# Kernel tuning notes

Hardware: AMD Instinct MI355X
Metric: run time of the kernel (lower is better)

The kernel has to match this reference:

```python
import jax, jax.numpy as jnp
import numpy as np

D_MODEL = 1024
NUM_HEADS = 16
HEAD_DIM = D_MODEL // NUM_HEADS
THETA = 10000.0
B, T = 2, 2048


def setup_inputs() -> dict:
    key = jax.random.key(0)
    k1, k2, k3 = jax.random.split(key, 3)
    x = jax.random.normal(k1, (B, T, D_MODEL), dtype=jnp.float32)
    W_qkv = jax.random.normal(k2, (3 * D_MODEL, D_MODEL), dtype=jnp.float32) * 0.02
    W_o = jax.random.normal(k3, (D_MODEL, D_MODEL), dtype=jnp.float32) * 0.02
    return {"x": x, "W_qkv": W_qkv, "W_o": W_o}


def _rope(x, cos, sin):
    # x: [B, h, T, d]; rotate interleaved even/odd pairs
    x_even = x[..., 0::2]
    x_odd = x[..., 1::2]
    out_even = x_even * cos - x_odd * sin
    out_odd = x_even * sin + x_odd * cos
    out = jnp.stack([out_even, out_odd], axis=-1)  # [B,h,T,d/2,2]
    return out.reshape(x.shape)


def reference(x, W_qkv, W_o):
    b, t, dm = x.shape
    # fused QKV projection (bias-free Linear: x @ W.T)
    qkv = jnp.einsum('btd,ed->bte', x, W_qkv)                # [B,T,3*D]
    qkv = qkv.reshape(b, t, 3, NUM_HEADS, HEAD_DIM)
    qkv = jnp.transpose(qkv, (2, 0, 3, 1, 4))                # [3,B,h,T,d]
    q, k, v = qkv[0], qkv[1], qkv[2]

    # RoPE with token_positions = arange(T)
    pos = jnp.arange(t, dtype=jnp.float32)                   # [T]
    inv_freq = THETA ** (-jnp.arange(0, HEAD_DIM, 2, dtype=jnp.float32) / HEAD_DIM)
    ang = pos[:, None] * inv_freq[None, :]                   # [T, d/2]
    cos = jnp.cos(ang)[None, None, :, :]
    sin = jnp.sin(ang)[None, None, :, :]
    q = _rope(q, cos, sin)
    k = _rope(k, cos, sin)

    # causal scaled dot-product attention
    scale = 1.0 / jnp.sqrt(jnp.asarray(HEAD_DIM, dtype=x.dtype))
    scores = jnp.einsum('bhqd,bhkd->bhqk', q, k) * scale     # [B,h,T,T]
    causal = jnp.tril(jnp.ones((t, t), dtype=bool))
    scores = jnp.where(causal[None, None, :, :], scores, -jnp.inf)
    attn = jax.nn.softmax(scores, axis=-1)
    out = jnp.einsum('bhqk,bhkd->bhqd', attn, v)             # [B,h,T,d]
    out = jnp.transpose(out, (0, 2, 1, 3)).reshape(b, t, dm) # [B,T,D]
    return jnp.einsum('btd,ed->bte', out, W_o)
```

## Files before the change

### kernel.cpp

```cpp
#include <hip/hip_runtime.h>
#include <hip/hip_bf16.h>
#include <cstdint>

#define NHEADS 16
#define HDIM 64
#define BB 2
#define TSEQ 2048
#define DM 1024
#define MROWS (BB*TSEQ)

typedef unsigned short u16;
typedef unsigned int u32;
typedef __bf16 bf16x8 __attribute__((ext_vector_type(8)));
typedef float f32x4 __attribute__((ext_vector_type(4)));

#define AS1C(p) ((const __attribute__((address_space(1))) u32*)(p))
#define AS3(p)  ((__attribute__((address_space(3))) u32*)(p))

static __device__ __forceinline__ u16 f2bf(float f) {
  return __builtin_bit_cast(u16, __float2bfloat16(f));
}
static __device__ __forceinline__ float bf2f(u16 u) {
  return __bfloat162float(__builtin_bit_cast(__hip_bfloat16, u));
}
static __device__ __forceinline__ u32 pack2bf(float a, float b) {
  const u32 ua = __builtin_bit_cast(u32, a) + 0x8000u;
  const u32 ub = __builtin_bit_cast(u32, b) + 0x8000u;
  return (ua >> 16) | (ub & 0xFFFF0000u);
}
static __device__ __forceinline__ f32x4 mfma16x16(bf16x8 a, bf16x8 b, f32x4 c) {
  return __builtin_amdgcn_mfma_f32_16x16x32_bf16(a, b, c, 0, 0, 0);
}

#define N4_X   (MROWS * DM / 4)
#define N4_WQ  (3 * DM * DM / 4)
#define N4_WO  (DM * DM / 4)
__global__ __launch_bounds__(256) void cast_all(const float* __restrict__ x,
                                                const float* __restrict__ wq,
                                                const float* __restrict__ wo,
                                                u16* __restrict__ xb,
                                                u16* __restrict__ wqb,
                                                u16* __restrict__ wob) {
  int i = blockIdx.x * 256 + threadIdx.x;
  const int stride = gridDim.x * 256;
  for (; i < N4_X + N4_WQ + N4_WO; i += stride) {
    const float4* src; u16* dst; int j;
    if (i < N4_X)            { src = (const float4*)x;  dst = xb;  j = i; }
    else if (i < N4_X + N4_WQ) { src = (const float4*)wq; dst = wqb; j = i - N4_X; }
    else                     { src = (const float4*)wo; dst = wob; j = i - N4_X - N4_WQ; }
    float4 v = src[j];
    ushort4 o;
    o.x = f2bf(v.x); o.y = f2bf(v.y); o.z = f2bf(v.z); o.w = f2bf(v.w);
    ((ushort4*)dst)[j] = o;
  }
}

template<int WRITE_BF16>
__global__ __launch_bounds__(256, 2) void gemm_bt(const u16* __restrict__ A,
                                                  const u16* __restrict__ Bm,
                                                  float* __restrict__ Cf,
                                                  u16* __restrict__ Cb,
                                                  int M, int N, int K) {
  __shared__ u16 lA[2][128 * 32];
  __shared__ u16 lB[2][128 * 32];
  const int tid = threadIdx.x;
  const int w = tid >> 6, l = tid & 63;
  const int wr = w >> 1, wc = w & 1;
  int bid = blockIdx.y * gridDim.x + blockIdx.x;
  const int cpx = (gridDim.x * gridDim.y) >> 3;
  bid = (bid & 7) * cpx + (bid >> 3);
  const int bx = bid % gridDim.x, by = bid / gridDim.x;
  const int brow = by * 128, bcol = bx * 128;
  const int lr = l & 15, lg = l >> 4;

  const int srow = l >> 2;
  const int scol = (((l & 3) ^ (srow & 3)) * 8);

  auto stage = [&](int buf, int k0) {
#pragma unroll
    for (int is = 0; is < 2; ++is) {
      const int chunk = w * 2 + is;
      const int row = chunk * 16 + srow;
      __builtin_amdgcn_global_load_lds(AS1C(A + (size_t)(brow + row) * K + k0 + scol),
                                       AS3((char*)lA[buf] + chunk * 1024), 16, 0, 0);
      __builtin_amdgcn_global_load_lds(AS1C(Bm + (size_t)(bcol + row) * K + k0 + scol),
                                       AS3((char*)lB[buf] + chunk * 1024), 16, 0, 0);
    }
  };

  f32x4 acc[4][4] = {};
  const int nk = K >> 5;
  stage(0, 0);
  for (int kk = 0; kk < nk; ++kk) {
    const int cur = kk & 1;
    __syncthreads();
    if (kk + 1 < nk) stage(cur ^ 1, (kk + 1) << 5);
    bf16x8 af[4], bfr[4];
#pragma unroll
    for (int m = 0; m < 4; ++m) {
      const int row = wr * 64 + m * 16 + lr;
      const int sl = lg ^ (row & 3);
      af[m] = *(const bf16x8*)(&lA[cur][row * 32 + sl * 8]);
    }
#pragma unroll
    for (int n = 0; n < 4; ++n) {
      const int row = wc * 64 + n * 16 + lr;
      const int sl = lg ^ (row & 3);
      bfr[n] = *(const bf16x8*)(&lB[cur][row * 32 + sl * 8]);
    }
#pragma unroll
    for (int m = 0; m < 4; ++m)
#pragma unroll
      for (int n = 0; n < 4; ++n)
        acc[m][n] = mfma16x16(af[m], bfr[n], acc[m][n]);
  }
#pragma unroll
  for (int m = 0; m < 4; ++m)
#pragma unroll
    for (int n = 0; n < 4; ++n)
#pragma unroll
      for (int r = 0; r < 4; ++r) {
        const int row = brow + wr * 64 + m * 16 + lg * 4 + r;
        const int col = bcol + wc * 64 + n * 16 + lr;
        if constexpr (WRITE_BF16)
          Cb[(size_t)row * N + col] = f2bf(acc[m][n][r]);
        else
          Cf[(size_t)row * N + col] = acc[m][n][r];
      }
}

__global__ __launch_bounds__(256, 2) void gemm_bt64(const u16* __restrict__ A,
                                                    const u16* __restrict__ Bm,
                                                    float* __restrict__ Cf,
                                                    int M, int N, int K) {
  __shared__ u16 lA[2][64 * 32];
  __shared__ u16 lB[2][128 * 32];
  const int tid = threadIdx.x;
  const int w = tid >> 6, l = tid & 63;
  const int wr = w >> 1, wc = w & 1;
  int bid = blockIdx.y * gridDim.x + blockIdx.x;
  const int cpx = (gridDim.x * gridDim.y) >> 3;
  bid = (bid & 7) * cpx + (bid >> 3);
  const int bx = bid % gridDim.x, by = bid / gridDim.x;
  const int brow = by * 64, bcol = bx * 128;
  const int lr = l & 15, lg = l >> 4;

  const int srow = l >> 2;
  const int scol = (((l & 3) ^ (srow & 3)) * 8);

  auto stage = [&](int buf, int k0) {
    {
      const int row = w * 16 + srow;
      __builtin_amdgcn_global_load_lds(AS1C(A + (size_t)(brow + row) * K + k0 + scol),
                                       AS3((char*)lA[buf] + w * 1024), 16, 0, 0);
    }
#pragma unroll
    for (int is = 0; is < 2; ++is) {
      const int chunk = w * 2 + is;
      const int row = chunk * 16 + srow;
      __builtin_amdgcn_global_load_lds(AS1C(Bm + (size_t)(bcol + row) * K + k0 + scol),
                                       AS3((char*)lB[buf] + chunk * 1024), 16, 0, 0);
    }
  };

  f32x4 acc[2][4] = {};
  const int nk = K >> 5;
  stage(0, 0);
  for (int kk = 0; kk < nk; ++kk) {
    const int cur = kk & 1;
    __syncthreads();
    if (kk + 1 < nk) stage(cur ^ 1, (kk + 1) << 5);
    bf16x8 af[2], bfr[4];
#pragma unroll
    for (int m = 0; m < 2; ++m) {
      const int row = wr * 32 + m * 16 + lr;
      const int sl = lg ^ (row & 3);
      af[m] = *(const bf16x8*)(&lA[cur][row * 32 + sl * 8]);
    }
#pragma unroll
    for (int n = 0; n < 4; ++n) {
      const int row = wc * 64 + n * 16 + lr;
      const int sl = lg ^ (row & 3);
      bfr[n] = *(const bf16x8*)(&lB[cur][row * 32 + sl * 8]);
    }
#pragma unroll
    for (int m = 0; m < 2; ++m)
#pragma unroll
      for (int n = 0; n < 4; ++n)
        acc[m][n] = mfma16x16(af[m], bfr[n], acc[m][n]);
  }
#pragma unroll
  for (int m = 0; m < 2; ++m)
#pragma unroll
    for (int n = 0; n < 4; ++n)
#pragma unroll
      for (int r = 0; r < 4; ++r) {
        const int row = brow + wr * 32 + m * 16 + lg * 4 + r;
        const int col = bcol + wc * 64 + n * 16 + lr;
        Cf[(size_t)row * N + col] = acc[m][n][r];
      }
}

__global__ __launch_bounds__(256) void rope_reshape(const u16* __restrict__ qkvb,
                                                    u16* __restrict__ qb,
                                                    u16* __restrict__ kb,
                                                    u16* __restrict__ vbT) {
  const int bh = blockIdx.y;
  const int b = bh >> 4, h = bh & 15;
  const int t0 = blockIdx.x * 64;
  const int tid = threadIdx.x;
  const float C = -0.4152410118609203f;
  const float QS = 0.125f * 1.44269504088896341f;
  const float R2PI = 0.15915494309189535f;

  for (int idx = tid; idx < 64 * 8; idx += 256) {
    const int tl = idx >> 3, grp = idx & 7;
    const int t = t0 + tl;
    const size_t base = ((size_t)(b * TSEQ + t)) * 3072 + h * 64 + grp * 8;
    u16 qv[8], kv8[8], qo[8], ko[8];
    *(uint4*)qv  = *(const uint4*)(qkvb + base);
    *(uint4*)kv8 = *(const uint4*)(qkvb + base + 1024);
#pragma unroll
    for (int j = 0; j < 4; ++j) {
      const int p = grp * 4 + j;
      const float inv = exp2f((float)p * C);
      const float rev = __builtin_amdgcn_fractf((float)t * inv * R2PI);
      const float sn = __builtin_amdgcn_sinf(rev);
      const float cs = __builtin_amdgcn_cosf(rev);
      const float qe = bf2f(qv[2 * j]), qoo = bf2f(qv[2 * j + 1]);
      const float ke = bf2f(kv8[2 * j]), koo = bf2f(kv8[2 * j + 1]);
      qo[2 * j]     = f2bf((qe * cs - qoo * sn) * QS);
      qo[2 * j + 1] = f2bf((qe * sn + qoo * cs) * QS);
      ko[2 * j]     = f2bf(ke * cs - koo * sn);
      ko[2 * j + 1] = f2bf(ke * sn + koo * cs);
    }
    const size_t obase = ((size_t)bh * TSEQ + t) * 64 + grp * 8;
    *(uint4*)(qb + obase) = *(uint4*)qo;
    *(uint4*)(kb + obase) = *(uint4*)ko;
  }

  __shared__ u16 lT[64][65];
  for (int idx = tid; idx < 64 * 64; idx += 256) {
    const int tl = idx >> 6, d = idx & 63;
    lT[tl][d] = qkvb[((size_t)(b * TSEQ + t0 + tl)) * 3072 + 2048 + h * 64 + d];
  }
  __syncthreads();
  for (int idx = tid; idx < 64 * 64; idx += 256) {
    const int d = idx >> 6, tl = idx & 63;
    vbT[((size_t)bh * 64 + d) * TSEQ + t0 + tl] = lT[tl][d];
  }
}

__global__ __launch_bounds__(512, 4) void attn_fwd(const u16* __restrict__ qb,
                                                   const u16* __restrict__ kb,
                                                   const u16* __restrict__ vbT,
                                                   u16* __restrict__ ob) {
  __shared__ u16 lK[4][64 * 64];
  __shared__ u16 lV[4][64 * 64];
  __shared__ u16 lP[8][16 * 64];
  const int hw = blockIdx.x;
  const int logical = (hw & 7) * 64 + (hw >> 3);
  const int bh = logical >> 4;
  const int pair = logical & 15;
  const int b = bh >> 4, h = bh & 15;
  const int tid = threadIdx.x;
  const int w = tid >> 6, l = tid & 63;
  const int g = w >> 2, wq = w & 3;
  const int lr = l & 15, lg = l >> 4;
  const int srow8 = l >> 3;
  const int scol = ((l & 7) ^ srow8) * 8;
  const u16* Kb = kb + (size_t)bh * TSEQ * 64;
  const u16* Vb = vbT + (size_t)bh * 64 * TSEQ;
  u16* lPw = lP[w];

  auto stage = [&](int buf, int kt) {
#pragma unroll
    for (int is = 0; is < 2; ++is) {
      const int chunk = wq * 2 + is;
      const int row = chunk * 8 + srow8;
      __builtin_amdgcn_global_load_lds(AS1C(Kb + (size_t)(kt * 64 + row) * 64 + scol),
                                       AS3((char*)lK[buf] + chunk * 1024), 16, 0, 0);
      __builtin_amdgcn_global_load_lds(AS1C(Vb + (size_t)row * TSEQ + kt * 64 + scol),
                                       AS3((char*)lV[buf] + chunk * 1024), 16, 0, 0);
    }
  };

  for (int half = 0; half < 2; ++half) {
    const int qt = half ? (TSEQ / 64 - 1 - pair) : pair;
    const int q0 = qt * 64;

    bf16x8 qf[2];
    {
      const u16* qp = qb + ((size_t)bh * TSEQ + q0 + wq * 16 + lr) * 64 + lg * 8;
      qf[0] = *(const bf16x8*)qp;
      qf[1] = *(const bf16x8*)(qp + 32);
    }

    f32x4 oacc[4] = {};
    float lsum = 0.f;

    const int nt = qt + 1;
    const int nit = (nt + 1) >> 1;
    const int ql = wq * 16 + lr;

    __syncthreads();
    if (g < nt) stage(g * 2, g);
    for (int it = 0; it < nit; ++it) {
      const int cur = it & 1;
      __syncthreads();
      const int ktn = 2 * (it + 1) + g;
      if (ktn < nt) stage(g * 2 + (cur ^ 1), ktn);
      const int kt = 2 * it + g;
      if (kt < nt) {
        const u16* Kc = lK[g * 2 + cur];
        const u16* Vc = lV[g * 2 + cur];

        f32x4 s[4] = {};
        __builtin_amdgcn_s_setprio(1);
#pragma unroll
        for (int n = 0; n < 4; ++n) {
          const int row = n * 16 + lr;
#pragma unroll
          for (int ks = 0; ks < 2; ++ks) {
            const int sl = (ks * 4 + lg) ^ (row & 7);
            bf16x8 kf = *(const bf16x8*)(&Kc[row * 64 + sl * 8]);
            s[n] = mfma16x16(kf, qf[ks], s[n]);
          }
        }
        __builtin_amdgcn_s_setprio(0);

        const bool diag = (kt == qt);
#pragma unroll
        for (int n = 0; n < 4; ++n) {
          float pv[4];
#pragma unroll
          for (int r = 0; r < 4; ++r) {
            float p = __builtin_amdgcn_exp2f(s[n][r]);
            if (diag && (n * 16 + lg * 4 + r > ql)) p = 0.f;
            pv[r] = p;
            lsum += p;
          }
          const u32 w0 = pack2bf(pv[0], pv[1]);
          const u32 w1 = pack2bf(pv[2], pv[3]);
          const int phys = (n * 2 + (lg >> 1)) ^ (lr & 7);
          uint2 pk; pk.x = w0; pk.y = w1;
          *(uint2*)(&lPw[lr * 64 + phys * 8 + (lg & 1) * 4]) = pk;
        }

        bf16x8 pf[2];
#pragma unroll
        for (int ks = 0; ks < 2; ++ks) {
          const int phys = (ks * 4 + lg) ^ (lr & 7);
          pf[ks] = *(const bf16x8*)(&lPw[lr * 64 + phys * 8]);
        }
        __builtin_amdgcn_s_setprio(1);
#pragma unroll
        for (int n = 0; n < 4; ++n) {
          const int row = n * 16 + lr;
#pragma unroll
          for (int ks = 0; ks < 2; ++ks) {
            const int sl = (ks * 4 + lg) ^ (row & 7);
            bf16x8 vf = *(const bf16x8*)(&Vc[row * 64 + sl * 8]);
            oacc[n] = mfma16x16(vf, pf[ks], oacc[n]);
          }
        }
        __builtin_amdgcn_s_setprio(0);
      }
    }

    lsum += __shfl_xor(lsum, 16);
    lsum += __shfl_xor(lsum, 32);

    __syncthreads();
    float* mO = (float*)&lK[0][0];
    float* mL = (float*)&lV[0][0];
    if (g == 1) {
#pragma unroll
      for (int n = 0; n < 4; ++n)
#pragma unroll
        for (int r = 0; r < 4; ++r) {
          const int d = n * 16 + lg * 4 + r;
          mO[wq * 1024 + d * 16 + lr] = oacc[n][r];
        }
      if (lg == 0) mL[wq * 16 + lr] = lsum;
    }
    __syncthreads();
    if (g == 0) {
      const float rl = 1.f / (lsum + mL[wq * 16 + lr]);
      const int q = q0 + wq * 16 + lr;
#pragma unroll
      for (int n = 0; n < 4; ++n) {
        ushort4 ov;
#pragma unroll
        for (int r = 0; r < 4; ++r) {
          const int d = n * 16 + lg * 4 + r;
          const float o = oacc[n][r] + mO[wq * 1024 + d * 16 + lr];
          ((u16*)&ov)[r] = f2bf(o * rl);
        }
        *(ushort4*)(&ob[(size_t)(b * TSEQ + q) * DM + h * 64 + n * 16 + lg * 4]) = ov;
      }
    }
  }
}

extern "C" void kernel_launch(void* const* d_in, const int* in_sizes, int n_in,
                              void* d_out, int out_size, void* d_ws, size_t ws_size,
                              hipStream_t stream) {
  const float* x    = (const float*)d_in[0];
  const float* Wqkv = (const float*)d_in[1];
  const float* Wo   = (const float*)d_in[2];
  float* out = (float*)d_out;

  char* ws = (char*)d_ws;
  u16* xb    = (u16*)ws; ws += (size_t)MROWS * DM * 2;
  u16* wqkvb = (u16*)ws; ws += (size_t)3 * DM * DM * 2;
  u16* wob   = (u16*)ws; ws += (size_t)DM * DM * 2;
  u16* qkvb  = (u16*)ws; ws += (size_t)MROWS * 3 * DM * 2;
  u16* qb    = (u16*)ws; ws += (size_t)BB * NHEADS * TSEQ * HDIM * 2;
  u16* kb    = (u16*)ws; ws += (size_t)BB * NHEADS * TSEQ * HDIM * 2;
  u16* vbT   = (u16*)ws; ws += (size_t)BB * NHEADS * TSEQ * HDIM * 2;
  u16* ob    = (u16*)ws; ws += (size_t)MROWS * DM * 2;

  cast_all<<<2048, 256, 0, stream>>>(x, Wqkv, Wo, xb, wqkvb, wob);

  gemm_bt<1><<<dim3(3 * DM / 128, MROWS / 128), 256, 0, stream>>>(
      xb, wqkvb, nullptr, qkvb, MROWS, 3 * DM, DM);

  rope_reshape<<<dim3(TSEQ / 64, BB * NHEADS), 256, 0, stream>>>(qkvb, qb, kb, vbT);

  attn_fwd<<<512, 512, 0, stream>>>(qb, kb, vbT, ob);

  gemm_bt64<<<dim3(DM / 128, MROWS / 64), 256, 0, stream>>>(
      ob, wob, out, MROWS, DM, DM);
}
```

Baseline: 106.7 us.

## Fuse RoPE, head reshape and V transpose into QKV GEMM epilogue

The separate rope_reshape kernel and the intermediate qkv bf16 buffer are removed. The QKV GEMM epilogue now applies RoPE (with the softmax scale folded into Q) using a lane shuffle to fetch each pair partner, and writes Q and K directly in per-head layout. V is written transposed as packed 4-element stores. This saves one kernel launch and a full write/read round trip of the QKV tensor. In exchange the GEMM epilogue does more transcendental math and scattered stores, which lengthens the GEMM.

After: 100.6 us. 5.7% less time.

```diff
diff --git a/kernel.cpp b/kernel.cpp
--- a/kernel.cpp
+++ b/kernel.cpp
@@ -55,12 +55,12 @@
   }
 }
 
-template<int WRITE_BF16>
-__global__ __launch_bounds__(256, 2) void gemm_bt(const u16* __restrict__ A,
-                                                  const u16* __restrict__ Bm,
-                                                  float* __restrict__ Cf,
-                                                  u16* __restrict__ Cb,
-                                                  int M, int N, int K) {
+__global__ __launch_bounds__(256, 2) void gemm_qkv(const u16* __restrict__ A,
+                                                   const u16* __restrict__ Bm,
+                                                   u16* __restrict__ qb,
+                                                   u16* __restrict__ kbuf,
+                                                   u16* __restrict__ vbT,
+                                                   int M, int N, int K) {
   __shared__ u16 lA[2][128 * 32];
   __shared__ u16 lB[2][128 * 32];
   const int tid = threadIdx.x;
@@ -114,19 +114,52 @@
       for (int n = 0; n < 4; ++n)
         acc[m][n] = mfma16x16(af[m], bfr[n], acc[m][n]);
   }
-#pragma unroll
-  for (int m = 0; m < 4; ++m)
-#pragma unroll
-    for (int n = 0; n < 4; ++n)
-#pragma unroll
-      for (int r = 0; r < 4; ++r) {
-        const int row = brow + wr * 64 + m * 16 + lg * 4 + r;
-        const int col = bcol + wc * 64 + n * 16 + lr;
-        if constexpr (WRITE_BF16)
-          Cb[(size_t)row * N + col] = f2bf(acc[m][n][r]);
-        else
-          Cf[(size_t)row * N + col] = acc[m][n][r];
+
+  const float C = -0.4152410118609203f;
+  const float QS = 0.125f * 1.44269504088896341f;
+  const float R2PI = 0.15915494309189535f;
+
+  if (bcol < 2048) {
+    const bool isq = (bcol < 1024);
+    const int head = ((bcol + wc * 64) >> 6) & 15;
+    u16* dst = isq ? qb : kbuf;
+#pragma unroll
+    for (int n = 0; n < 4; ++n) {
+      const int d = n * 16 + lr;
+      const float inv = exp2f((float)(d >> 1) * C);
+#pragma unroll
+      for (int m = 0; m < 4; ++m)
+#pragma unroll
+        for (int r = 0; r < 4; ++r) {
+          const int row = brow + wr * 64 + m * 16 + lg * 4 + r;
+          const int t = row & (TSEQ - 1), b = row >> 11;
+          const float own = acc[m][n][r];
+          const float oth = __shfl_xor(own, 1);
+          const float rev = __builtin_amdgcn_fractf((float)t * inv * R2PI);
+          float sn = __builtin_amdgcn_sinf(rev);
+          float cs = __builtin_amdgcn_cosf(rev);
+          if (isq) { sn *= QS; cs *= QS; }
+          const float out = (lr & 1) ? (oth * sn + own * cs)
+                                     : (own * cs - oth * sn);
+          dst[(((size_t)(b * 16 + head)) * TSEQ + t) * 64 + d] = f2bf(out);
+        }
+    }
+  } else {
+    const int head = (((bcol - 2048) + wc * 64) >> 6) & 15;
+#pragma unroll
+    for (int n = 0; n < 4; ++n) {
+      const int d = n * 16 + lr;
+#pragma unroll
+      for (int m = 0; m < 4; ++m) {
+        const int row0 = brow + wr * 64 + m * 16 + lg * 4;
+        const int t = row0 & (TSEQ - 1), b = row0 >> 11;
+        uint2 pk;
+        pk.x = pack2bf(acc[m][n][0], acc[m][n][1]);
+        pk.y = pack2bf(acc[m][n][2], acc[m][n][3]);
+        *(uint2*)(&vbT[((size_t)(b * 16 + head) * 64 + d) * TSEQ + t]) = pk;
       }
+    }
+  }
 }
 
 __global__ __launch_bounds__(256, 2) void gemm_bt64(const u16* __restrict__ A,
@@ -199,56 +232,6 @@
         const int col = bcol + wc * 64 + n * 16 + lr;
         Cf[(size_t)row * N + col] = acc[m][n][r];
       }
-}
-
-__global__ __launch_bounds__(256) void rope_reshape(const u16* __restrict__ qkvb,
-                                                    u16* __restrict__ qb,
-                                                    u16* __restrict__ kb,
-                                                    u16* __restrict__ vbT) {
-  const int bh = blockIdx.y;
-  const int b = bh >> 4, h = bh & 15;
-  const int t0 = blockIdx.x * 64;
-  const int tid = threadIdx.x;
-  const float C = -0.4152410118609203f;
-  const float QS = 0.125f * 1.44269504088896341f;
-  const float R2PI = 0.15915494309189535f;
-
-  for (int idx = tid; idx < 64 * 8; idx += 256) {
-    const int tl = idx >> 3, grp = idx & 7;
-    const int t = t0 + tl;
-    const size_t base = ((size_t)(b * TSEQ + t)) * 3072 + h * 64 + grp * 8;
-    u16 qv[8], kv8[8], qo[8], ko[8];
-    *(uint4*)qv  = *(const uint4*)(qkvb + base);
-    *(uint4*)kv8 = *(const uint4*)(qkvb + base + 1024);
-#pragma unroll
-    for (int j = 0; j < 4; ++j) {
-      const int p = grp * 4 + j;
-      const float inv = exp2f((float)p * C);
-      const float rev = __builtin_amdgcn_fractf((float)t * inv * R2PI);
-      const float sn = __builtin_amdgcn_sinf(rev);
-      const float cs = __builtin_amdgcn_cosf(rev);
-      const float qe = bf2f(qv[2 * j]), qoo = bf2f(qv[2 * j + 1]);
-      const float ke = bf2f(kv8[2 * j]), koo = bf2f(kv8[2 * j + 1]);
-      qo[2 * j]     = f2bf((qe * cs - qoo * sn) * QS);
-      qo[2 * j + 1] = f2bf((qe * sn + qoo * cs) * QS);
-      ko[2 * j]     = f2bf(ke * cs - koo * sn);
-      ko[2 * j + 1] = f2bf(ke * sn + koo * cs);
-    }
-    const size_t obase = ((size_t)bh * TSEQ + t) * 64 + grp * 8;
-    *(uint4*)(qb + obase) = *(uint4*)qo;
-    *(uint4*)(kb + obase) = *(uint4*)ko;
-  }
-
-  __shared__ u16 lT[64][65];
-  for (int idx = tid; idx < 64 * 64; idx += 256) {
-    const int tl = idx >> 6, d = idx & 63;
-    lT[tl][d] = qkvb[((size_t)(b * TSEQ + t0 + tl)) * 3072 + 2048 + h * 64 + d];
-  }
-  __syncthreads();
-  for (int idx = tid; idx < 64 * 64; idx += 256) {
-    const int d = idx >> 6, tl = idx & 63;
-    vbT[((size_t)bh * 64 + d) * TSEQ + t0 + tl] = lT[tl][d];
-  }
 }
 
 __global__ __launch_bounds__(512, 4) void attn_fwd(const u16* __restrict__ qb,
@@ -415,7 +398,6 @@
   u16* xb    = (u16*)ws; ws += (size_t)MROWS * DM * 2;
   u16* wqkvb = (u16*)ws; ws += (size_t)3 * DM * DM * 2;
   u16* wob   = (u16*)ws; ws += (size_t)DM * DM * 2;
-  u16* qkvb  = (u16*)ws; ws += (size_t)MROWS * 3 * DM * 2;
   u16* qb    = (u16*)ws; ws += (size_t)BB * NHEADS * TSEQ * HDIM * 2;
   u16* kb    = (u16*)ws; ws += (size_t)BB * NHEADS * TSEQ * HDIM * 2;
   u16* vbT   = (u16*)ws; ws += (size_t)BB * NHEADS * TSEQ * HDIM * 2;
@@ -423,10 +405,8 @@
 
   cast_all<<<2048, 256, 0, stream>>>(x, Wqkv, Wo, xb, wqkvb, wob);
 
-  gemm_bt<1><<<dim3(3 * DM / 128, MROWS / 128), 256, 0, stream>>>(
-      xb, wqkvb, nullptr, qkvb, MROWS, 3 * DM, DM);
-
-  rope_reshape<<<dim3(TSEQ / 64, BB * NHEADS), 256, 0, stream>>>(qkvb, qb, kb, vbT);
+  gemm_qkv<<<dim3(3 * DM / 128, MROWS / 128), 256, 0, stream>>>(
+      xb, wqkvb, qb, kb, vbT, MROWS, 3 * DM, DM);
 
   attn_fwd<<<512, 512, 0, stream>>>(qb, kb, vbT, ob);
 
```
